# Kernel optimization log

Measured on AMD Instinct MI355X. Metric: run time of the kernel, lower is better.

Reference implementation:

```python
import jax, jax.numpy as jnp
import numpy as np
import math

NP2 = 64      # number of RF pulses
V = 32768     # number of voxels


def _shift_matrix(kmax):
    """EPG shift matrix, exact translation of EPG_shift_matrices."""
    N = 3 * (kmax + 1)
    S = np.zeros(N * N, dtype=np.complex64)
    kidx = list(range(3, N, 3)); sidx = [x - 3 for x in kidx]
    S[[a + N * b for a, b in zip(kidx, sidx)]] = 1
    kidx = list(range(4, N, 3)); kidx.pop(); sidx = [x + 3 for x in kidx]
    S[[a + N * b for a, b in zip(kidx, sidx)]] = 1
    kidx = list(range(2, N, 3))
    S[[a + N * b for a, b in zip(kidx, kidx)]] = 1
    S = S.reshape(N, N).T.copy()
    S[0:2, 4] = 1
    return jnp.asarray(S, dtype=jnp.complex64)


def _rf_rot_all(theta):
    """RF rotation matrices for all pulses at once. theta: [P] complex -> [P,3,3]."""
    a = jnp.abs(theta)
    phi = jnp.angle(theta)
    ca2 = (jnp.cos(a / 2) ** 2).astype(jnp.complex64)
    sa2 = jnp.sin(a / 2) ** 2
    sa = jnp.sin(a)
    ca = jnp.cos(a).astype(jnp.complex64)
    ep = jnp.exp(1j * phi)
    em = jnp.exp(-1j * phi)
    e2m = jnp.exp(-2j * phi)
    r00 = ca2
    r10 = e2m * sa2
    r20 = -0.5j * em * sa
    r01 = jnp.conj(r10)
    r11 = ca2
    r21 = 0.5j * ep * sa
    r02 = -1j * ep * sa
    r12 = 1j * em * sa
    r22 = ca
    row0 = jnp.stack([r00, r01, r02], axis=-1)
    row1 = jnp.stack([r10, r11, r12], axis=-1)
    row2 = jnp.stack([r20, r21, r22], axis=-1)
    return jnp.stack([row0, row1, row2], axis=-2).astype(jnp.complex64)


def _epg_gre_f0(theta, T1, T2, TR):
    """Single-compartment GRE EPG recurrence. Returns F0 signal [V, np2].

    Uses full-width (kmax) state updates every pulse: states beyond
    kmax_per_pulse are exactly zero on the ramp-up and cannot influence
    F0 on the ramp-down, so F0 matches the variable-width torch loop.
    """
    np2 = theta.shape[0]
    kmax = np2 - 1
    kpp_max = math.ceil(np2 / 2)
    if kpp_max < kmax:
        kmax = kpp_max
    K = kmax + 1
    N = 3 * K
    v = T1.shape[0]

    St = _shift_matrix(kmax).T                      # [N,N], so S @ f == f @ St
    E1 = jnp.exp(-TR / T1)[:, 0]                    # [V]
    E2 = jnp.exp(-TR / T2)[:, 0]                    # [V]
    # diagonal of kron(I_K, diag(E2,E2,E1)) per voxel -> [V,N]
    e = jnp.tile(jnp.stack([E2, E2, E1], axis=1), (1, K)).astype(jnp.complex64)
    b = jnp.zeros((v, N), jnp.complex64).at[:, 2].set((1 - E1).astype(jnp.complex64))

    A_all = _rf_rot_all(theta)                      # [np2,3,3]
    FF0 = jnp.zeros((v, N), jnp.complex64).at[:, 2].set(1.0)

    def step(FF, A):
        # block-diag kron(I_K, A) applied to the state vector
        Fcol = jnp.einsum('ab,vkb->vka', A, FF.reshape(v, K, 3)).reshape(v, N)
        # relaxation * shift + recovery
        FFn = e * (Fcol @ St) + b
        FFn = FFn.at[:, 0].set(jnp.conj(FFn[:, 0]))
        return FFn, Fcol[:, 0]

    _, F0 = jax.lax.scan(step, FF0, A_all)          # F0: [np2, V]
    return F0.T                                     # [V, np2]


def setup_inputs() -> dict:
    key = jax.random.key(0)
    k1, k2, k3, k4, k5 = jax.random.split(key, 5)
    flip = jax.random.uniform(k1, (NP2,), minval=0.1, maxval=math.pi / 2)
    phase = jax.random.uniform(k2, (NP2,), minval=-math.pi, maxval=math.pi)
    theta_re = (flip * jnp.cos(phase)).astype(jnp.float32)
    theta_im = (flip * jnp.sin(phase)).astype(jnp.float32)
    PD = jax.random.uniform(k3, (V, 1), minval=0.2, maxval=1.0)
    T1 = jax.random.uniform(k4, (V, 1), minval=300.0, maxval=1500.0)
    T2 = jax.random.uniform(k5, (V, 1), minval=20.0, maxval=120.0)
    qmaps = jnp.stack([PD, T1, T2], axis=0).astype(jnp.float32)  # [3,V,1]
    TR = jnp.array([10.0], jnp.float32)
    return {"theta_re": theta_re, "theta_im": theta_im, "TR": TR,
            "quantitative_maps": qmaps}


def reference(theta_re, theta_im, TR, quantitative_maps):
    theta = (theta_re + 1j * theta_im).astype(jnp.complex64)
    PD = quantitative_maps[0]   # [V,1]
    T1 = quantitative_maps[1]   # [V,1]
    T2 = quantitative_maps[2]   # [V,1]
    s = _epg_gre_f0(theta, T1, T2, TR)   # [V, np2] complex
    return jnp.abs(s) * PD
```

## Files before the change

kernel.cpp:

```cpp
#include <hip/hip_runtime.h>
#include <math.h>


#define NP2 64
#define ROR1  0x121
#define ROR15 0x12F

typedef float v2f __attribute__((ext_vector_type(2)));
typedef float v8f __attribute__((ext_vector_type(8)));

template<int CTRL>
__device__ __forceinline__ float rowrot(float x) {
    return __int_as_float(
        __builtin_amdgcn_mov_dpp(__float_as_int(x), CTRL, 0xF, 0xF, true));
}
__device__ __forceinline__ v2f mk2(float a, float b) { v2f r; r.x = a; r.y = b; return r; }

#define PAIR(V, i)  __builtin_shufflevector((V), (V), (i), (i) + 1)
#define FMA2(a, b, c) __builtin_elementwise_fma((a), (b), (c))

__global__ void coef_kernel(const float* __restrict__ theta_re,
                            const float* __restrict__ theta_im,
                            float* __restrict__ cw)
{
    const int t = threadIdx.x;
    if (t < NP2) {
        const float tre = theta_re[t], tim = theta_im[t];
        const float a2 = tre * tre + tim * tim;
        const float inva = __frsqrt_rn(a2);
        const float a = a2 * inva;
        const float c = tre * inva, s = tim * inva;
        float cp = 1.f, sp = 0.f;
        if (t > 0) {
            const float ure = theta_re[t - 1], uim = theta_im[t - 1];
            const float ia = __frsqrt_rn(ure * ure + uim * uim);
            cp = ure * ia; sp = uim * ia;
        }
        const float cd = cp * c + sp * s;
        const float sd = sp * c - cp * s;
        float sa, ca;
        __sincosf(a, &sa, &ca);
        const float ca2 = 0.5f + 0.5f * ca;
        const float sa2 = 0.5f - 0.5f * ca;
        const float h = 0.5f * sa;
        float4* row = (float4*)(cw + t * 16);
        row[0] = make_float4(cd, cd, sd, sd);
        row[1] = make_float4(ca2, ca2, sa2, sa2);
        row[2] = make_float4(sa, sa, ca, ca);
        row[3] = make_float4(h, h, 0.f, 0.f);
    } else if (t < NP2 + 4) {
        ((float4*)(cw + NP2 * 16))[t - NP2] = make_float4(0.f, 0.f, 0.f, 0.f);
    }
}

struct St { v2f Pr, Pi, Mr, Mi, Zr, Zi; };

__device__ __forceinline__ v2f step(St& S,
    v2f Ccd, v2f Csd, v2f Cca2, v2f Csa2, v2f Csa, v2f Cca, v2f Ch,
    v2f pE1, v2f pE2, v2f rec, bool s0, bool s15)
{
    const v2f ec = pE2 * Ccd, es = pE2 * Csd;
    const v2f hPr = FMA2(ec, S.Pr, -(es * S.Pi));
    const v2f hPi = FMA2(ec, S.Pi,  (es * S.Pr));
    const v2f hMr = FMA2(ec, S.Mr,  (es * S.Mi));
    const v2f hMi = FMA2(ec, S.Mi, -(es * S.Mr));
    const v2f ezr = FMA2(pE1, S.Zr, rec);
    const v2f ezi = pE1 * S.Zi;
    const v2f szr = Csa * ezr, szi = Csa * ezi;
    const v2f nPr = FMA2(Cca2, hPr, FMA2(Csa2, hMr,  szi));
    const v2f nPi = FMA2(Cca2, hPi, FMA2(Csa2, hMi, -szr));
    const v2f nMr = FMA2(Csa2, hPr, FMA2(Cca2, hMr, -szi));
    const v2f nMi = FMA2(Csa2, hPi, FMA2(Cca2, hMi,  szr));
    const v2f d1 = hPi - hMi, d2 = hMr - hPr;
    S.Zr = FMA2(Ch, d1, Cca * ezr);
    S.Zi = FMA2(Ch, d2, Cca * ezi);
    const float rPrx = rowrot<ROR1>(nPr.x),  rPry = rowrot<ROR1>(nPr.y);
    const float rPix = rowrot<ROR1>(nPi.x),  rPiy = rowrot<ROR1>(nPi.y);
    const float rMrx = rowrot<ROR15>(nMr.x), rMry = rowrot<ROR15>(nMr.y);
    const float rMix = rowrot<ROR15>(nMi.x), rMiy = rowrot<ROR15>(nMi.y);
    S.Pr.y = s0 ?  rPrx : rPry;
    S.Pi.y = s0 ?  rPix : rPiy;
    S.Pr.x = s0 ?  rMrx : rPrx;
    S.Pi.x = s0 ? -rMix : rPix;
    S.Mr.x = s15 ? rMry : rMrx;
    S.Mi.x = s15 ? rMiy : rMix;
    S.Mr.y = s15 ? 0.f : rMry;
    S.Mi.y = s15 ? 0.f : rMiy;
    return mk2(nPr.x, nPi.x);
}

__global__ __launch_bounds__(256, 8) void epg_kernel(
    const float* __restrict__ TRp,
    const float* __restrict__ qmaps,
    const float* __restrict__ cw,
    float* __restrict__ out, int V)
{
    const int t = threadIdx.x;
    const int sub = t & 15;
    const int vloc = t >> 4;
    const int vA = blockIdx.x * 32 + vloc;
    const int vB = vA + 16;

    __shared__ __align__(16) v2f bufc[32][65];

    const float tr = TRp[0];
    const float E1A = __expf(-tr / qmaps[V + vA]);
    const float E2A = __expf(-tr / qmaps[2 * V + vA]);
    const float E1B = __expf(-tr / qmaps[V + vB]);
    const float E2B = __expf(-tr / qmaps[2 * V + vB]);
    const bool s0 = (sub == 0);
    const bool s15 = (sub == 15);
    const v2f pE1A = mk2(E1A, E1A), pE2A = mk2(E2A, E2A);
    const v2f pE1B = mk2(E1B, E1B), pE2B = mk2(E2B, E2B);
    const v2f recA = mk2(s0 ? (1.f - E1A) : 0.f, 0.f);
    const v2f recB = mk2(s0 ? (1.f - E1B) : 0.f, 0.f);

    St A, B;
    A.Pr = mk2(0.f, 0.f); A.Pi = A.Pr; A.Mr = A.Pr; A.Mi = A.Pr; A.Zr = A.Pr; A.Zi = A.Pr;
    B = A;
    if (s0) { A.Zr.x = 1.0f; B.Zr.x = 1.0f; }

    v8f A0, A1, B0, B1;
    asm volatile("s_load_dwordx8 %0, %1, 0x0"  : "=s"(B0) : "s"(cw));
    asm volatile("s_load_dwordx8 %0, %1, 0x20" : "=s"(B1) : "s"(cw));
    asm volatile("s_waitcnt lgkmcnt(0)"
                 : "=s"(A0), "=s"(A1) : "0"(B0), "1"(B1));

#pragma unroll 1
    for (int p = 0; p < NP2; ++p) {
        const float* nx = cw + (p + 1) * 16;
        asm volatile("s_load_dwordx8 %0, %1, 0x0"  : "=s"(B0) : "s"(nx));
        asm volatile("s_load_dwordx8 %0, %1, 0x20" : "=s"(B1) : "s"(nx));

        const v2f Ccd  = PAIR(A0, 0), Csd  = PAIR(A0, 2);
        const v2f Cca2 = PAIR(A0, 4), Csa2 = PAIR(A0, 6);
        const v2f Csa  = PAIR(A1, 0), Cca  = PAIR(A1, 2), Ch = PAIR(A1, 4);

        const v2f f0a = step(A, Ccd, Csd, Cca2, Csa2, Csa, Cca, Ch,
                             pE1A, pE2A, recA, s0, s15);
        const v2f f0b = step(B, Ccd, Csd, Cca2, Csa2, Csa, Cca, Ch,
                             pE1B, pE2B, recB, s0, s15);
        if (s0) {
            bufc[vloc][p] = f0a;
            bufc[vloc + 16][p] = f0b;
        }

        asm volatile("s_waitcnt lgkmcnt(0)"
                     : "=s"(A0), "=s"(A1) : "0"(B0), "1"(B1));
    }

    __syncthreads();
    float4* out4 = (float4*)out;
#pragma unroll
    for (int i = 0; i < 2; ++i) {
        const int q = i * 256 + t;
        const int r = q >> 4;
        const int c = (q & 15) * 4;
        const float PDr = qmaps[blockIdx.x * 32 + r];
        const v2f a = bufc[r][c],     b = bufc[r][c + 1];
        const v2f d = bufc[r][c + 2], e = bufc[r][c + 3];
        float4 val;
        val.x = sqrtf(a.x * a.x + a.y * a.y) * PDr;
        val.y = sqrtf(b.x * b.x + b.y * b.y) * PDr;
        val.z = sqrtf(d.x * d.x + d.y * d.y) * PDr;
        val.w = sqrtf(e.x * e.x + e.y * e.y) * PDr;
        out4[blockIdx.x * 512 + q] = val;
    }
}

extern "C" void kernel_launch(void* const* d_in, const int* in_sizes, int n_in,
                              void* d_out, int out_size, void* d_ws, size_t ws_size,
                              hipStream_t stream) {
    const float* theta_re = (const float*)d_in[0];
    const float* theta_im = (const float*)d_in[1];
    const float* TRp      = (const float*)d_in[2];
    const float* qmaps    = (const float*)d_in[3];
    float* out = (float*)d_out;
    float* cw  = (float*)d_ws;
    const int V = in_sizes[3] / 3;
    coef_kernel<<<dim3(1), dim3(128), 0, stream>>>(theta_re, theta_im, cw);
    epg_kernel<<<dim3(V / 32), dim3(256), 0, stream>>>(TRp, qmaps, cw, out, V);
}
```

Before: 108.6 us.

## Run EPG recurrence in packed fp16 and skip empty state slots on ramp phases

```diff
diff --git a/kernel.cpp b/kernel.cpp
--- a/kernel.cpp
+++ b/kernel.cpp
@@ -1,27 +1,27 @@
 #include <hip/hip_runtime.h>
+#include <hip/hip_fp16.h>
 #include <math.h>
 
 
 #define NP2 64
 #define ROR1  0x121
 #define ROR15 0x12F
-
-typedef float v2f __attribute__((ext_vector_type(2)));
-typedef float v8f __attribute__((ext_vector_type(8)));
-
+#define RSHL1 0x101
+
+__device__ __forceinline__ unsigned h2u(__half2 x) {
+    unsigned u; __builtin_memcpy(&u, &x, 4); return u;
+}
+__device__ __forceinline__ __half2 u2h(unsigned u) {
+    __half2 h; __builtin_memcpy(&h, &u, 4); return h;
+}
 template<int CTRL>
-__device__ __forceinline__ float rowrot(float x) {
-    return __int_as_float(
-        __builtin_amdgcn_mov_dpp(__float_as_int(x), CTRL, 0xF, 0xF, true));
-}
-__device__ __forceinline__ v2f mk2(float a, float b) { v2f r; r.x = a; r.y = b; return r; }
-
-#define PAIR(V, i)  __builtin_shufflevector((V), (V), (i), (i) + 1)
-#define FMA2(a, b, c) __builtin_elementwise_fma((a), (b), (c))
+__device__ __forceinline__ __half2 rroth(__half2 x) {
+    return u2h((unsigned)__builtin_amdgcn_mov_dpp((int)h2u(x), CTRL, 0xF, 0xF, true));
+}
 
 __global__ void coef_kernel(const float* __restrict__ theta_re,
                             const float* __restrict__ theta_im,
-                            float* __restrict__ cw)
+                            unsigned* __restrict__ cw)
 {
     const int t = threadIdx.x;
     if (t < NP2) {
@@ -42,57 +42,48 @@
         __sincosf(a, &sa, &ca);
         const float ca2 = 0.5f + 0.5f * ca;
         const float sa2 = 0.5f - 0.5f * ca;
-        const float h = 0.5f * sa;
-        float4* row = (float4*)(cw + t * 16);
-        row[0] = make_float4(cd, cd, sd, sd);
-        row[1] = make_float4(ca2, ca2, sa2, sa2);
-        row[2] = make_float4(sa, sa, ca, ca);
-        row[3] = make_float4(h, h, 0.f, 0.f);
-    } else if (t < NP2 + 4) {
-        ((float4*)(cw + NP2 * 16))[t - NP2] = make_float4(0.f, 0.f, 0.f, 0.f);
-    }
-}
-
-struct St { v2f Pr, Pi, Mr, Mi, Zr, Zi; };
-
-__device__ __forceinline__ v2f step(St& S,
-    v2f Ccd, v2f Csd, v2f Cca2, v2f Csa2, v2f Csa, v2f Cca, v2f Ch,
-    v2f pE1, v2f pE2, v2f rec, bool s0, bool s15)
+        unsigned* row = cw + t * 8;
+        const float vals[8] = { cd, sd, ca2, sa2, sa, ca, 0.5f * sa, 0.f };
+        for (int j = 0; j < 8; ++j) {
+            const __half h = __float2half(vals[j]);
+            __half2 hp = __halves2half2(h, h);
+            unsigned u; __builtin_memcpy(&u, &hp, 4);
+            row[j] = u;
+        }
+    } else if (t < NP2 + 8) {
+        cw[NP2 * 8 + (t - NP2)] = 0u;
+    }
+}
+
+__device__ __forceinline__ void slot_mat(
+    __half2 Pr, __half2 Pi, __half2 Mr, __half2 Mi, __half2& Zr, __half2& Zi,
+    __half2 ec, __half2 es, __half2 esn,
+    __half2 ca2, __half2 sa2, __half2 sa, __half2 ca, __half2 hh,
+    __half2 pE1, __half2 rec,
+    __half2& nPr, __half2& nPi, __half2& nMr, __half2& nMi)
 {
-    const v2f ec = pE2 * Ccd, es = pE2 * Csd;
-    const v2f hPr = FMA2(ec, S.Pr, -(es * S.Pi));
-    const v2f hPi = FMA2(ec, S.Pi,  (es * S.Pr));
-    const v2f hMr = FMA2(ec, S.Mr,  (es * S.Mi));
-    const v2f hMi = FMA2(ec, S.Mi, -(es * S.Mr));
-    const v2f ezr = FMA2(pE1, S.Zr, rec);
-    const v2f ezi = pE1 * S.Zi;
-    const v2f szr = Csa * ezr, szi = Csa * ezi;
-    const v2f nPr = FMA2(Cca2, hPr, FMA2(Csa2, hMr,  szi));
-    const v2f nPi = FMA2(Cca2, hPi, FMA2(Csa2, hMi, -szr));
-    const v2f nMr = FMA2(Csa2, hPr, FMA2(Cca2, hMr, -szi));
-    const v2f nMi = FMA2(Csa2, hPi, FMA2(Cca2, hMi,  szr));
-    const v2f d1 = hPi - hMi, d2 = hMr - hPr;
-    S.Zr = FMA2(Ch, d1, Cca * ezr);
-    S.Zi = FMA2(Ch, d2, Cca * ezi);
-    const float rPrx = rowrot<ROR1>(nPr.x),  rPry = rowrot<ROR1>(nPr.y);
-    const float rPix = rowrot<ROR1>(nPi.x),  rPiy = rowrot<ROR1>(nPi.y);
-    const float rMrx = rowrot<ROR15>(nMr.x), rMry = rowrot<ROR15>(nMr.y);
-    const float rMix = rowrot<ROR15>(nMi.x), rMiy = rowrot<ROR15>(nMi.y);
-    S.Pr.y = s0 ?  rPrx : rPry;
-    S.Pi.y = s0 ?  rPix : rPiy;
-    S.Pr.x = s0 ?  rMrx : rPrx;
-    S.Pi.x = s0 ? -rMix : rPix;
-    S.Mr.x = s15 ? rMry : rMrx;
-    S.Mi.x = s15 ? rMiy : rMix;
-    S.Mr.y = s15 ? 0.f : rMry;
-    S.Mi.y = s15 ? 0.f : rMiy;
-    return mk2(nPr.x, nPi.x);
+    const __half2 hPr = __hfma2(ec, Pr, __hmul2(esn, Pi));
+    const __half2 hPi = __hfma2(ec, Pi, __hmul2(es,  Pr));
+    const __half2 hMr = __hfma2(ec, Mr, __hmul2(es,  Mi));
+    const __half2 hMi = __hfma2(ec, Mi, __hmul2(esn, Mr));
+    const __half2 ezr = __hfma2(pE1, Zr, rec);
+    const __half2 ezi = __hmul2(pE1, Zi);
+    const __half2 szr = __hmul2(sa, ezr);
+    const __half2 szi = __hmul2(sa, ezi);
+    const __half2 szrn = __hneg2(szr);
+    const __half2 szin = __hneg2(szi);
+    nPr = __hfma2(ca2, hPr, __hfma2(sa2, hMr, szi));
+    nPi = __hfma2(ca2, hPi, __hfma2(sa2, hMi, szrn));
+    nMr = __hfma2(sa2, hPr, __hfma2(ca2, hMr, szin));
+    nMi = __hfma2(sa2, hPi, __hfma2(ca2, hMi, szr));
+    Zr = __hfma2(hh, __hsub2(hPi, hMi), __hmul2(ca, ezr));
+    Zi = __hfma2(hh, __hsub2(hMr, hPr), __hmul2(ca, ezi));
 }
 
 __global__ __launch_bounds__(256, 8) void epg_kernel(
     const float* __restrict__ TRp,
     const float* __restrict__ qmaps,
-    const float* __restrict__ cw,
+    const unsigned* __restrict__ cw,
     float* __restrict__ out, int V)
 {
     const int t = threadIdx.x;
@@ -101,7 +92,7 @@
     const int vA = blockIdx.x * 32 + vloc;
     const int vB = vA + 16;
 
-    __shared__ __align__(16) v2f bufc[32][65];
+    __shared__ unsigned bufPr[16][65], bufPi[16][65];
 
     const float tr = TRp[0];
     const float E1A = __expf(-tr / qmaps[V + vA]);
@@ -110,43 +101,92 @@
     const float E2B = __expf(-tr / qmaps[2 * V + vB]);
     const bool s0 = (sub == 0);
     const bool s15 = (sub == 15);
-    const v2f pE1A = mk2(E1A, E1A), pE2A = mk2(E2A, E2A);
-    const v2f pE1B = mk2(E1B, E1B), pE2B = mk2(E2B, E2B);
-    const v2f recA = mk2(s0 ? (1.f - E1A) : 0.f, 0.f);
-    const v2f recB = mk2(s0 ? (1.f - E1B) : 0.f, 0.f);
-
-    St A, B;
-    A.Pr = mk2(0.f, 0.f); A.Pi = A.Pr; A.Mr = A.Pr; A.Mi = A.Pr; A.Zr = A.Pr; A.Zi = A.Pr;
-    B = A;
-    if (s0) { A.Zr.x = 1.0f; B.Zr.x = 1.0f; }
-
-    v8f A0, A1, B0, B1;
-    asm volatile("s_load_dwordx8 %0, %1, 0x0"  : "=s"(B0) : "s"(cw));
-    asm volatile("s_load_dwordx8 %0, %1, 0x20" : "=s"(B1) : "s"(cw));
-    asm volatile("s_waitcnt lgkmcnt(0)"
-                 : "=s"(A0), "=s"(A1) : "0"(B0), "1"(B1));
+    const __half2 pE1 = __floats2half2_rn(E1A, E1B);
+    const __half2 pE2 = __floats2half2_rn(E2A, E2B);
+    const __half2 zeroH = __floats2half2_rn(0.f, 0.f);
+    const __half2 recH = s0 ? __floats2half2_rn(1.f - E1A, 1.f - E1B) : zeroH;
+
+    __half2 Pr0 = zeroH, Pr1 = zeroH, Pi0 = zeroH, Pi1 = zeroH;
+    __half2 Mr0 = zeroH, Mr1 = zeroH, Mi0 = zeroH, Mi1 = zeroH;
+    __half2 Zr0 = s0 ? __floats2half2_rn(1.f, 1.f) : zeroH;
+    __half2 Zr1 = zeroH, Zi0 = zeroH, Zi1 = zeroH;
+
+    const uint4* __restrict__ cwq = (const uint4*)cw;
+    uint4 q0 = cwq[0], q1 = cwq[1];
+
+    __half2 nPr0, nPi0, nMr0, nMi0, nPr1, nPi1, nMr1, nMi1;
 
 #pragma unroll 1
-    for (int p = 0; p < NP2; ++p) {
-        const float* nx = cw + (p + 1) * 16;
-        asm volatile("s_load_dwordx8 %0, %1, 0x0"  : "=s"(B0) : "s"(nx));
-        asm volatile("s_load_dwordx8 %0, %1, 0x20" : "=s"(B1) : "s"(nx));
-
-        const v2f Ccd  = PAIR(A0, 0), Csd  = PAIR(A0, 2);
-        const v2f Cca2 = PAIR(A0, 4), Csa2 = PAIR(A0, 6);
-        const v2f Csa  = PAIR(A1, 0), Cca  = PAIR(A1, 2), Ch = PAIR(A1, 4);
-
-        const v2f f0a = step(A, Ccd, Csd, Cca2, Csa2, Csa, Cca, Ch,
-                             pE1A, pE2A, recA, s0, s15);
-        const v2f f0b = step(B, Ccd, Csd, Cca2, Csa2, Csa, Cca, Ch,
-                             pE1B, pE2B, recB, s0, s15);
-        if (s0) {
-            bufc[vloc][p] = f0a;
-            bufc[vloc + 16][p] = f0b;
-        }
-
-        asm volatile("s_waitcnt lgkmcnt(0)"
-                     : "=s"(A0), "=s"(A1) : "0"(B0), "1"(B1));
+    for (int p = 0; p < 15; ++p) {
+        const int nb = 2 * (p + 1);
+        const uint4 n0 = cwq[nb], n1 = cwq[nb + 1];
+        const __half2 ec = __hmul2(pE2, u2h(q0.x));
+        const __half2 es = __hmul2(pE2, u2h(q0.y));
+        const __half2 esn = __hneg2(es);
+        slot_mat(Pr0, Pi0, Mr0, Mi0, Zr0, Zi0, ec, es, esn,
+                 u2h(q0.z), u2h(q0.w), u2h(q1.x), u2h(q1.y), u2h(q1.z),
+                 pE1, recH, nPr0, nPi0, nMr0, nMi0);
+        if (s0) { bufPr[vloc][p] = h2u(nPr0); bufPi[vloc][p] = h2u(nPi0); }
+        const __half2 rPr = rroth<ROR1>(nPr0);
+        const __half2 rPi = rroth<ROR1>(nPi0);
+        const __half2 rMr = rroth<RSHL1>(nMr0);
+        const __half2 rMi = rroth<RSHL1>(nMi0);
+        Pr0 = s0 ? rMr : rPr;
+        Pi0 = s0 ? __hneg2(rMi) : rPi;
+        Mr0 = rMr;
+        Mi0 = rMi;
+        q0 = n0; q1 = n1;
+    }
+
+#pragma unroll 1
+    for (int p = 15; p < 48; ++p) {
+        const int nb = 2 * (p + 1);
+        const uint4 n0 = cwq[nb], n1 = cwq[nb + 1];
+        const __half2 ec = __hmul2(pE2, u2h(q0.x));
+        const __half2 es = __hmul2(pE2, u2h(q0.y));
+        const __half2 esn = __hneg2(es);
+        const __half2 ca2 = u2h(q0.z), sa2 = u2h(q0.w);
+        const __half2 sa = u2h(q1.x), ca = u2h(q1.y), hh = u2h(q1.z);
+        slot_mat(Pr0, Pi0, Mr0, Mi0, Zr0, Zi0, ec, es, esn,
+                 ca2, sa2, sa, ca, hh, pE1, recH, nPr0, nPi0, nMr0, nMi0);
+        slot_mat(Pr1, Pi1, Mr1, Mi1, Zr1, Zi1, ec, es, esn,
+                 ca2, sa2, sa, ca, hh, pE1, zeroH, nPr1, nPi1, nMr1, nMi1);
+        if (s0) { bufPr[vloc][p] = h2u(nPr0); bufPi[vloc][p] = h2u(nPi0); }
+        const __half2 rPr0 = rroth<ROR1>(nPr0),  rPr1 = rroth<ROR1>(nPr1);
+        const __half2 rPi0 = rroth<ROR1>(nPi0),  rPi1 = rroth<ROR1>(nPi1);
+        const __half2 rMr0 = rroth<ROR15>(nMr0), rMr1 = rroth<ROR15>(nMr1);
+        const __half2 rMi0 = rroth<ROR15>(nMi0), rMi1 = rroth<ROR15>(nMi1);
+        Pr1 = s0 ? rPr0 : rPr1;
+        Pi1 = s0 ? rPi0 : rPi1;
+        Pr0 = s0 ? rMr0 : rPr0;
+        Pi0 = s0 ? __hneg2(rMi0) : rPi0;
+        Mr0 = s15 ? rMr1 : rMr0;
+        Mi0 = s15 ? rMi1 : rMi0;
+        Mr1 = s15 ? zeroH : rMr1;
+        Mi1 = s15 ? zeroH : rMi1;
+        q0 = n0; q1 = n1;
+    }
+
+#pragma unroll 1
+    for (int p = 48; p < NP2; ++p) {
+        const int nb = 2 * (p + 1);
+        const uint4 n0 = cwq[nb], n1 = cwq[nb + 1];
+        const __half2 ec = __hmul2(pE2, u2h(q0.x));
+        const __half2 es = __hmul2(pE2, u2h(q0.y));
+        const __half2 esn = __hneg2(es);
+        slot_mat(Pr0, Pi0, Mr0, Mi0, Zr0, Zi0, ec, es, esn,
+                 u2h(q0.z), u2h(q0.w), u2h(q1.x), u2h(q1.y), u2h(q1.z),
+                 pE1, recH, nPr0, nPi0, nMr0, nMi0);
+        if (s0) { bufPr[vloc][p] = h2u(nPr0); bufPi[vloc][p] = h2u(nPi0); }
+        const __half2 rPr = rroth<ROR1>(nPr0);
+        const __half2 rPi = rroth<ROR1>(nPi0);
+        const __half2 rMr = rroth<RSHL1>(nMr0);
+        const __half2 rMi = rroth<RSHL1>(nMi0);
+        Pr0 = s0 ? rMr : rPr;
+        Pi0 = s0 ? __hneg2(rMi) : rPi;
+        Mr0 = rMr;
+        Mi0 = rMi;
+        q0 = n0; q1 = n1;
     }
 
     __syncthreads();
@@ -156,14 +196,19 @@
         const int q = i * 256 + t;
         const int r = q >> 4;
         const int c = (q & 15) * 4;
+        const int row = r & 15;
+        const bool hi = (r >> 4) != 0;
         const float PDr = qmaps[blockIdx.x * 32 + r];
-        const v2f a = bufc[r][c],     b = bufc[r][c + 1];
-        const v2f d = bufc[r][c + 2], e = bufc[r][c + 3];
         float4 val;
-        val.x = sqrtf(a.x * a.x + a.y * a.y) * PDr;
-        val.y = sqrtf(b.x * b.x + b.y * b.y) * PDr;
-        val.z = sqrtf(d.x * d.x + d.y * d.y) * PDr;
-        val.w = sqrtf(e.x * e.x + e.y * e.y) * PDr;
+        float* vp = &val.x;
+#pragma unroll
+        for (int j = 0; j < 4; ++j) {
+            const __half2 hr = u2h(bufPr[row][c + j]);
+            const __half2 hii = u2h(bufPi[row][c + j]);
+            const float pr = hi ? __high2float(hr) : __low2float(hr);
+            const float pi = hi ? __high2float(hii) : __low2float(hii);
+            vp[j] = sqrtf(pr * pr + pi * pi) * PDr;
+        }
         out4[blockIdx.x * 512 + q] = val;
     }
 }
@@ -176,7 +221,7 @@
     const float* TRp      = (const float*)d_in[2];
     const float* qmaps    = (const float*)d_in[3];
     float* out = (float*)d_out;
-    float* cw  = (float*)d_ws;
+    unsigned* cw = (unsigned*)d_ws;
     const int V = in_sizes[3] / 3;
     coef_kernel<<<dim3(1), dim3(128), 0, stream>>>(theta_re, theta_im, cw);
     epg_kernel<<<dim3(V / 32), dim3(256), 0, stream>>>(TRp, qmaps, cw, out, V);
```

New measurement: 98.29 us. 9.5% less time.
